# Performance work log

Measured on AMD Instinct MI355X. Metric: run time of the kernel, lower is better.

Reference implementation:

```python
import jax, jax.numpy as jnp
import numpy as np

K = 5  # kernel_size

def _extract_patches(x):
    # TF extract_patches, SAME padding, stride 1, rate 1.
    # x: (B,H,W,C) -> (B,H,W,K*K,C); patch index i is row-major over (kh,kw),
    # channel d is the fastest-varying dim, matching TF's flatten order.
    p = K // 2
    xp = jnp.pad(x, ((0, 0), (p, p), (p, p), (0, 0)))
    B, H, W, C = x.shape
    pats = [xp[:, i:i + H, j:j + W, :] for i in range(K) for j in range(K)]
    return jnp.stack(pats, axis=3)

def setup_inputs() -> dict:
    key = jax.random.key(0)
    k1, k2, k3, k4 = jax.random.split(key, 4)
    B, H, W, C, F = 8, 250, 250, 4, 16
    return {
        "x": jax.random.normal(k1, (B, H, W, C), jnp.float32),
        "kernel": jax.random.normal(k2, (K, K, C, F), jnp.float32) * 0.05,
        "quad_kernel": jax.random.normal(k3, (C, K * K, K * K, F), jnp.float32) * 0.02,
        "bias": jax.random.normal(k4, (F,), jnp.float32) * 0.01,
    }

def reference(x, kernel, quad_kernel, bias):
    # Quadratic (Volterra) term: V[b,h,w,o] = sum_{i,j,d} p[bhwid] p[bhwjd] W[d,i,j,o]
    # (einsum 'abcid,abcjd,dijo->abcdo' followed by reduce_sum over d).
    patches = _extract_patches(x)  # (B,H,W,25,C)
    C = x.shape[-1]
    quad = 0.0
    for d in range(C):  # small fixed channel loop avoids a (B,H,W,25,C,F) intermediate
        pd = patches[..., d]                                   # (B,H,W,25)
        s = jnp.einsum('bhwj,ijo->bhwio', pd, quad_kernel[d])  # (B,H,W,25,F)
        quad = quad + jnp.einsum('bhwi,bhwio->bhwo', pd, s)    # (B,H,W,F)
    # Linear conv term (SAME padding, stride 1)
    lin = jax.lax.conv_general_dilated(
        x, kernel, window_strides=(1, 1), padding='SAME',
        dimension_numbers=('NHWC', 'HWIO', 'NHWC'))
    return quad + lin + bias
```

## Files before the change

kernel.cpp:

```cpp
#include <hip/hip_runtime.h>
#include <utility>


typedef _Float16 half2 __attribute__((ext_vector_type(2)));
typedef _Float16 half4 __attribute__((ext_vector_type(4)));
typedef _Float16 half8 __attribute__((ext_vector_type(8)));
typedef float floatx4 __attribute__((ext_vector_type(4)));

#define BB 8
#define HH 250
#define WW 250
#define NF 16
#define NSLOT_PAIR 181
#define NSLOT_LIN  13
#define NCHUNK     49
#define NFRAG      (NCHUNK * 64)

#define TW 32
#define TH 16
#define XW (TW + 4)
#define XH (TH + 4)
#define XSZ (XW * XH)

#define NBLK     512
#define NTILE_W  8
#define NTILE_H  16
#define NTILES   (BB * NTILE_H * NTILE_W)
#define NT       (NTILES / NBLK)

__host__ __device__ constexpr int slot_i(int s) {
    int i = 0, base = 0;
    while (base + (13 - (i >> 1)) <= s) { base += 13 - (i >> 1); ++i; }
    return i;
}
__host__ __device__ constexpr int slot_g(int s) {
    int i = 0, base = 0;
    while (base + (13 - (i >> 1)) <= s) { base += 13 - (i >> 1); ++i; }
    return (i >> 1) + (s - base);
}

__global__ void prep_frags(const float* __restrict__ lin_w,
                           const float* __restrict__ quad_w,
                           _Float16* __restrict__ fragB) {
    const int c = blockIdx.x;
    const int lane = threadIdx.x;
    const int n = lane & 15;
    const int d = lane >> 4;
    half8 frag;
    #pragma unroll
    for (int e = 0; e < 8; ++e) {
        const int f = c * 8 + e;
        const int s = f >> 1, hf = f & 1;
        float v = 0.f;
        if (s < NSLOT_PAIR) {
            int i = 0, base = 0;
            while (base + (13 - (i >> 1)) <= s) { base += 13 - (i >> 1); ++i; }
            const int g = (i >> 1) + (s - base);
            const int j = 2 * g + hf;
            if (j == i)
                v = quad_w[((d * 25 + i) * 25 + i) * 16 + n];
            else if (j > i && j < 25)
                v = quad_w[((d * 25 + i) * 25 + j) * 16 + n]
                  + quad_w[((d * 25 + j) * 25 + i) * 16 + n];
        } else if (s < NSLOT_PAIR + NSLOT_LIN) {
            const int j = 2 * (s - NSLOT_PAIR) + hf;
            if (j < 25) v = lin_w[(j * 4 + d) * 16 + n];
        }
        frag[e] = (_Float16)v;
    }
    *(half8*)(fragB + (c * 64 + lane) * 8) = frag;
}

__device__ __forceinline__ half2 pk(float lo, float hi) {
    return __builtin_bit_cast(half2, __builtin_amdgcn_cvt_pkrtz(lo, hi));
}

template<int S>
__device__ __forceinline__ half2 slotval(const half2 (&pd2)[13]) {
    if constexpr (S < NSLOT_PAIR) {
        constexpr int i = slot_i(S), g = slot_g(S);
        constexpr int ir = i >> 1, ih = i & 1;
        const half2 src = pd2[ir];
        const half2 bi = {src[ih], src[ih]};
        return bi * pd2[g];
    } else if constexpr (S < NSLOT_PAIR + NSLOT_LIN) {
        return pd2[S - NSLOT_PAIR];
    } else {
        return half2{(_Float16)0.f, (_Float16)0.f};
    }
}

template<int C>
__device__ __forceinline__ half8 make_frag(const half2 (&pd2)[13]) {
    const half2 a0 = slotval<C * 4 + 0>(pd2);
    const half2 a1 = slotval<C * 4 + 1>(pd2);
    const half2 a2 = slotval<C * 4 + 2>(pd2);
    const half2 a3 = slotval<C * 4 + 3>(pd2);
    const half4 lo = __builtin_shufflevector(a0, a1, 0, 1, 2, 3);
    const half4 hi = __builtin_shufflevector(a2, a3, 0, 1, 2, 3);
    return __builtin_shufflevector(lo, hi, 0, 1, 2, 3, 4, 5, 6, 7);
}

template<size_t... Cs>
__device__ __forceinline__ void gemm_all(
    const half2 (&p0)[13], const half2 (&p1)[13],
    const half2 (&p2)[13], const half2 (&p3)[13],
    const _Float16* sBlane,
    floatx4& a0, floatx4& a1, floatx4& a2, floatx4& a3,
    std::index_sequence<Cs...>) {
    (([&] {
        constexpr int C = (int)Cs;
        const half8 bf = *(const half8*)(sBlane + C * 64 * 8);
        a0 = __builtin_amdgcn_mfma_f32_16x16x32_f16(make_frag<C>(p0), bf, a0, 0, 0, 0);
        a1 = __builtin_amdgcn_mfma_f32_16x16x32_f16(make_frag<C>(p1), bf, a1, 0, 0, 0);
        a2 = __builtin_amdgcn_mfma_f32_16x16x32_f16(make_frag<C>(p2), bf, a2, 0, 0, 0);
        a3 = __builtin_amdgcn_mfma_f32_16x16x32_f16(make_frag<C>(p3), bf, a3, 0, 0, 0);
    }()), ...);
}

__device__ __forceinline__ void patches_from_window(const float* xt, int base,
                                                    half2 (&pdT)[13], half2 (&pdB)[13]) {
    float t6[6][5];
    #pragma unroll
    for (int rr = 0; rr < 6; ++rr)
        #pragma unroll
        for (int cc = 0; cc < 5; ++cc)
            t6[rr][cc] = xt[base + rr * XW + cc];

    float pf0[26], pf1[26];
    pf0[25] = 0.f; pf1[25] = 0.f;
    #pragma unroll
    for (int rr = 0; rr < 5; ++rr)
        #pragma unroll
        for (int cc = 0; cc < 5; ++cc) {
            pf0[rr * 5 + cc] = t6[rr][cc];
            pf1[rr * 5 + cc] = t6[rr + 1][cc];
        }
    #pragma unroll
    for (int t = 0; t < 13; ++t) {
        pdT[t] = pk(pf0[2 * t], pf0[2 * t + 1]);
        pdB[t] = pk(pf1[2 * t], pf1[2 * t + 1]);
    }
}

__device__ __forceinline__ void tile_coords(int T, int& b, int& h0, int& w0) {
    b = T >> 7;
    const int rem = T & 127;
    h0 = (rem >> 3) * TH;
    w0 = (rem & 7) * TW;
}

__device__ __forceinline__ void xload_regs(const float* __restrict__ x,
                                           int b, int h0, int w0,
                                           float4& v0, float4& v1) {
    const int p0 = threadIdx.x;
    {
        const int hh = p0 / XW, ww = p0 % XW;
        const int r = h0 + hh - 2, c = w0 + ww - 2;
        v0 = make_float4(0.f, 0.f, 0.f, 0.f);
        if (p0 < XSZ && (unsigned)r < (unsigned)HH && (unsigned)c < (unsigned)WW)
            v0 = ((const float4*)x)[(b * HH + r) * WW + c];
    }
    const int p1 = p0 + 512;
    v1 = make_float4(0.f, 0.f, 0.f, 0.f);
    if (p1 < XSZ) {
        const int hh = p1 / XW, ww = p1 % XW;
        const int r = h0 + hh - 2, c = w0 + ww - 2;
        if ((unsigned)r < (unsigned)HH && (unsigned)c < (unsigned)WW)
            v1 = ((const float4*)x)[(b * HH + r) * WW + c];
    }
}

__device__ __forceinline__ void xwrite_lds(float* xt, const float4& v0, const float4& v1) {
    const int p0 = threadIdx.x;
    if (p0 < XSZ) {
        xt[0 * XSZ + p0] = v0.x;
        xt[1 * XSZ + p0] = v0.y;
        xt[2 * XSZ + p0] = v0.z;
        xt[3 * XSZ + p0] = v0.w;
    }
    const int p1 = p0 + 512;
    if (p1 < XSZ) {
        xt[0 * XSZ + p1] = v1.x;
        xt[1 * XSZ + p1] = v1.y;
        xt[2 * XSZ + p1] = v1.z;
        xt[3 * XSZ + p1] = v1.w;
    }
}

__global__ __launch_bounds__(512, 4) void convquad_gemm(
    const float* __restrict__ x,
    const float* __restrict__ bias,
    const _Float16* __restrict__ fragB,
    float* __restrict__ out)
{
    __shared__ float xt[4 * XSZ];
    __shared__ __align__(16) _Float16 sB[NFRAG * 8];

    const int lane = threadIdx.x & 63;
    const int wv = threadIdx.x >> 6;
    const int m = lane & 15;
    const int q = lane >> 4;
    const float bo = bias[m];

    int b, h0, w0;
    tile_coords(blockIdx.x, b, h0, w0);
    float4 v0, v1;
    xload_regs(x, b, h0, w0, v0, v1);

    {
        const float4* src = (const float4*)fragB;
        float4* dst = (float4*)sB;
        #pragma unroll
        for (int t = threadIdx.x; t < NFRAG * 8 / 8; t += 512) dst[t] = src[t];
    }
    xwrite_lds(xt, v0, v1);
    __syncthreads();

    #pragma unroll 1
    for (int t = 0; t < NT; ++t) {
        int bn, h0n, w0n;
        if (t + 1 < NT) {
            tile_coords(blockIdx.x + (t + 1) * NBLK, bn, h0n, w0n);
            xload_regs(x, bn, h0n, w0n, v0, v1);
        }

        const int base = q * XSZ + (2 * wv) * XW + m;
        half2 pd0[13], pd1[13], pd2[13], pd3[13];
        patches_from_window(xt, base,      pd0, pd2);
        patches_from_window(xt, base + 16, pd1, pd3);

        floatx4 acc0 = {bo, bo, bo, bo};
        floatx4 acc1 = acc0, acc2 = acc0, acc3 = acc0;
        gemm_all(pd0, pd1, pd2, pd3, sB + lane * 8,
                 acc0, acc1, acc2, acc3, std::make_index_sequence<NCHUNK>{});

        const int r0 = h0 + 2 * wv;
        #pragma unroll
        for (int rr = 0; rr < 2; ++rr) {
            const int h = r0 + rr;
            if (h < HH) {
                const int rowbase = (b * HH + h) * WW;
                const floatx4& aA = rr ? acc2 : acc0;
                const floatx4& aB = rr ? acc3 : acc1;
                #pragma unroll
                for (int r = 0; r < 4; ++r) {
                    const int wA = w0 + q * 4 + r;
                    if (wA < WW) out[(rowbase + wA) * NF + m] = aA[r];
                    const int wB = w0 + 16 + q * 4 + r;
                    if (wB < WW) out[(rowbase + wB) * NF + m] = aB[r];
                }
            }
        }

        if (t + 1 < NT) {
            b = bn; h0 = h0n; w0 = w0n;
            __syncthreads();
            xwrite_lds(xt, v0, v1);
            __syncthreads();
        }
    }
}

extern "C" void kernel_launch(void* const* d_in, const int* in_sizes, int n_in,
                              void* d_out, int out_size, void* d_ws, size_t ws_size,
                              hipStream_t stream) {
    const float* x      = (const float*)d_in[0];
    const float* lin_w  = (const float*)d_in[1];
    const float* quad_w = (const float*)d_in[2];
    const float* bias   = (const float*)d_in[3];
    float* out = (float*)d_out;
    _Float16* fragB = (_Float16*)d_ws;

    prep_frags<<<dim3(NCHUNK), dim3(64), 0, stream>>>(lin_w, quad_w, fragB);

    convquad_gemm<<<dim3(NBLK), dim3(512), 0, stream>>>(x, bias, fragB, out);
}
```

Before: 102.5 us.

## Transpose input tile to column-major LDS and build patches with vector column loads

Changes the tile shape from 32x16 to 16x32 and stores the haloed input tile column-major in LDS. Each lane now reads 5 columns of 8 contiguous rows with float4 loads and builds patch vectors for 4 output rows, replacing many scalar LDS reads. The patch ordering becomes column-major, so the weight fragment preparation permutes the kernel indices to match. The goal is fewer LDS instructions and less patch-assembly work. The transposed LDS writes may cause bank conflicts.

```diff
diff --git a/kernel.cpp b/kernel.cpp
--- a/kernel.cpp
+++ b/kernel.cpp
@@ -16,15 +16,15 @@
 #define NCHUNK     49
 #define NFRAG      (NCHUNK * 64)
 
-#define TW 32
-#define TH 16
+#define TW 16
+#define TH 32
 #define XW (TW + 4)
 #define XH (TH + 4)
 #define XSZ (XW * XH)
 
 #define NBLK     512
-#define NTILE_W  8
-#define NTILE_H  16
+#define NTILE_W  16
+#define NTILE_H  8
 #define NTILES   (BB * NTILE_H * NTILE_W)
 #define NT       (NTILES / NBLK)
 
@@ -38,6 +38,7 @@
     while (base + (13 - (i >> 1)) <= s) { base += 13 - (i >> 1); ++i; }
     return (i >> 1) + (s - base);
 }
+__host__ __device__ constexpr int tr(int i) { return (i % 5) * 5 + (i / 5); }
 
 __global__ void prep_frags(const float* __restrict__ lin_w,
                            const float* __restrict__ quad_w,
@@ -58,13 +59,13 @@
             const int g = (i >> 1) + (s - base);
             const int j = 2 * g + hf;
             if (j == i)
-                v = quad_w[((d * 25 + i) * 25 + i) * 16 + n];
+                v = quad_w[((d * 25 + tr(i)) * 25 + tr(i)) * 16 + n];
             else if (j > i && j < 25)
-                v = quad_w[((d * 25 + i) * 25 + j) * 16 + n]
-                  + quad_w[((d * 25 + j) * 25 + i) * 16 + n];
+                v = quad_w[((d * 25 + tr(i)) * 25 + tr(j)) * 16 + n]
+                  + quad_w[((d * 25 + tr(j)) * 25 + tr(i)) * 16 + n];
         } else if (s < NSLOT_PAIR + NSLOT_LIN) {
             const int j = 2 * (s - NSLOT_PAIR) + hf;
-            if (j < 25) v = lin_w[(j * 4 + d) * 16 + n];
+            if (j < 25) v = lin_w[(tr(j) * 4 + d) * 16 + n];
         }
         frag[e] = (_Float16)v;
     }
@@ -118,36 +119,48 @@
     }()), ...);
 }
 
-__device__ __forceinline__ void patches_from_window(const float* xt, int base,
-                                                    half2 (&pdT)[13], half2 (&pdB)[13]) {
-    float t6[6][5];
+__device__ __forceinline__ void patches_cols(const float* xt, int base,
+                                             half2 (&pd)[4][13]) {
+    float carry[4];
     #pragma unroll
-    for (int rr = 0; rr < 6; ++rr)
+    for (int cc = 0; cc < 5; ++cc) {
+        const float4 lo = *(const float4*)(xt + base + cc * XH);
+        const float4 hi = *(const float4*)(xt + base + cc * XH + 4);
+        float col[8];
+        col[0] = lo.x; col[1] = lo.y; col[2] = lo.z; col[3] = lo.w;
+        col[4] = hi.x; col[5] = hi.y; col[6] = hi.z; col[7] = hi.w;
         #pragma unroll
-        for (int cc = 0; cc < 5; ++cc)
-            t6[rr][cc] = xt[base + rr * XW + cc];
-
-    float pf0[26], pf1[26];
-    pf0[25] = 0.f; pf1[25] = 0.f;
-    #pragma unroll
-    for (int rr = 0; rr < 5; ++rr)
-        #pragma unroll
-        for (int cc = 0; cc < 5; ++cc) {
-            pf0[rr * 5 + cc] = t6[rr][cc];
-            pf1[rr * 5 + cc] = t6[rr + 1][cc];
-        }
-    #pragma unroll
-    for (int t = 0; t < 13; ++t) {
-        pdT[t] = pk(pf0[2 * t], pf0[2 * t + 1]);
-        pdB[t] = pk(pf1[2 * t], pf1[2 * t + 1]);
+        for (int rr = 0; rr < 4; ++rr) {
+            if (cc == 0) {
+                pd[rr][0] = pk(col[0 + rr], col[1 + rr]);
+                pd[rr][1] = pk(col[2 + rr], col[3 + rr]);
+                carry[rr] = col[4 + rr];
+            } else if (cc == 1) {
+                pd[rr][2] = pk(carry[rr], col[0 + rr]);
+                pd[rr][3] = pk(col[1 + rr], col[2 + rr]);
+                pd[rr][4] = pk(col[3 + rr], col[4 + rr]);
+            } else if (cc == 2) {
+                pd[rr][5] = pk(col[0 + rr], col[1 + rr]);
+                pd[rr][6] = pk(col[2 + rr], col[3 + rr]);
+                carry[rr] = col[4 + rr];
+            } else if (cc == 3) {
+                pd[rr][7] = pk(carry[rr], col[0 + rr]);
+                pd[rr][8] = pk(col[1 + rr], col[2 + rr]);
+                pd[rr][9] = pk(col[3 + rr], col[4 + rr]);
+            } else {
+                pd[rr][10] = pk(col[0 + rr], col[1 + rr]);
+                pd[rr][11] = pk(col[2 + rr], col[3 + rr]);
+                pd[rr][12] = pk(col[4 + rr], 0.f);
+            }
+        }
     }
 }
 
 __device__ __forceinline__ void tile_coords(int T, int& b, int& h0, int& w0) {
     b = T >> 7;
     const int rem = T & 127;
-    h0 = (rem >> 3) * TH;
-    w0 = (rem & 7) * TW;
+    h0 = (rem >> 4) * TH;
+    w0 = (rem & 15) * TW;
 }
 
 __device__ __forceinline__ void xload_regs(const float* __restrict__ x,
@@ -174,17 +187,21 @@
 __device__ __forceinline__ void xwrite_lds(float* xt, const float4& v0, const float4& v1) {
     const int p0 = threadIdx.x;
     if (p0 < XSZ) {
-        xt[0 * XSZ + p0] = v0.x;
-        xt[1 * XSZ + p0] = v0.y;
-        xt[2 * XSZ + p0] = v0.z;
-        xt[3 * XSZ + p0] = v0.w;
+        const int hh = p0 / XW, ww = p0 % XW;
+        const int idx = ww * XH + hh;
+        xt[0 * XSZ + idx] = v0.x;
+        xt[1 * XSZ + idx] = v0.y;
+        xt[2 * XSZ + idx] = v0.z;
+        xt[3 * XSZ + idx] = v0.w;
     }
     const int p1 = p0 + 512;
     if (p1 < XSZ) {
-        xt[0 * XSZ + p1] = v1.x;
-        xt[1 * XSZ + p1] = v1.y;
-        xt[2 * XSZ + p1] = v1.z;
-        xt[3 * XSZ + p1] = v1.w;
+        const int hh = p1 / XW, ww = p1 % XW;
+        const int idx = ww * XH + hh;
+        xt[0 * XSZ + idx] = v1.x;
+        xt[1 * XSZ + idx] = v1.y;
+        xt[2 * XSZ + idx] = v1.z;
+        xt[3 * XSZ + idx] = v1.w;
     }
 }
 
@@ -194,7 +211,7 @@
     const _Float16* __restrict__ fragB,
     float* __restrict__ out)
 {
-    __shared__ float xt[4 * XSZ];
+    __shared__ __align__(16) float xt[4 * XSZ];
     __shared__ __align__(16) _Float16 sB[NFRAG * 8];
 
     const int lane = threadIdx.x & 63;
@@ -225,30 +242,27 @@
             xload_regs(x, bn, h0n, w0n, v0, v1);
         }
 
-        const int base = q * XSZ + (2 * wv) * XW + m;
-        half2 pd0[13], pd1[13], pd2[13], pd3[13];
-        patches_from_window(xt, base,      pd0, pd2);
-        patches_from_window(xt, base + 16, pd1, pd3);
+        const int base = q * XSZ + m * XH + 4 * wv;
+        half2 pd[4][13];
+        patches_cols(xt, base, pd);
 
         floatx4 acc0 = {bo, bo, bo, bo};
         floatx4 acc1 = acc0, acc2 = acc0, acc3 = acc0;
-        gemm_all(pd0, pd1, pd2, pd3, sB + lane * 8,
+        gemm_all(pd[0], pd[1], pd[2], pd[3], sB + lane * 8,
                  acc0, acc1, acc2, acc3, std::make_index_sequence<NCHUNK>{});
 
-        const int r0 = h0 + 2 * wv;
+        const int r0 = h0 + 4 * wv;
         #pragma unroll
-        for (int rr = 0; rr < 2; ++rr) {
+        for (int rr = 0; rr < 4; ++rr) {
             const int h = r0 + rr;
             if (h < HH) {
                 const int rowbase = (b * HH + h) * WW;
-                const floatx4& aA = rr ? acc2 : acc0;
-                const floatx4& aB = rr ? acc3 : acc1;
+                const floatx4& a = (rr == 0) ? acc0 : (rr == 1) ? acc1
+                                 : (rr == 2) ? acc2 : acc3;
                 #pragma unroll
                 for (int r = 0; r < 4; ++r) {
-                    const int wA = w0 + q * 4 + r;
-                    if (wA < WW) out[(rowbase + wA) * NF + m] = aA[r];
-                    const int wB = w0 + 16 + q * 4 + r;
-                    if (wB < WW) out[(rowbase + wB) * NF + m] = aB[r];
+                    const int w = w0 + q * 4 + r;
+                    if (w < WW) out[(rowbase + w) * NF + m] = a[r];
                 }
             }
         }
```

Result: slower. 111.4 us (+8.7%).
